# Optimization experiments

Measured on AMD Instinct MI355X. Metric: run time of the kernel, lower is better.

The kernel has to match this reference:

```python
import jax, jax.numpy as jnp
import numpy as np
import math

D_MODEL = 1024
NUM_HEADS = 16
HEAD_DIM = D_MODEL // NUM_HEADS
BATCH = 2
SEQ = 2048
THETA = 10000.0


def _rope_tables(seq_len, head_dim, theta=THETA):
    inv_freq = 1.0 / theta ** (jnp.arange(0, head_dim, 2, dtype=jnp.float32) / head_dim)
    pos = jnp.arange(seq_len, dtype=jnp.float32)
    freqs = jnp.outer(pos, inv_freq)                 # [S, hd/2]
    emb = jnp.concatenate([freqs, freqs], axis=-1)   # [S, hd]
    return jnp.cos(emb), jnp.sin(emb)


def _rotate_half(x):
    x1, x2 = jnp.split(x, 2, axis=-1)
    return jnp.concatenate([-x2, x1], axis=-1)


def setup_inputs() -> dict:
    key = jax.random.key(0)
    k1, k2, k3 = jax.random.split(key, 3)
    x = jax.random.normal(k1, (BATCH, SEQ, D_MODEL), dtype=jnp.float32)
    # causal mask: 1 where attend allowed, 0 where masked
    mask = jnp.tril(jnp.ones((SEQ, SEQ), dtype=jnp.int32))[None, None]
    w_qkv = jax.random.normal(k2, (D_MODEL, 3 * D_MODEL), dtype=jnp.float32) / math.sqrt(D_MODEL)
    w_out = jax.random.normal(k3, (D_MODEL, D_MODEL), dtype=jnp.float32) / math.sqrt(D_MODEL)
    return {"x": x, "mask": mask, "w_qkv": w_qkv, "w_out": w_out}


def reference(x, mask, w_qkv, w_out):
    B, S, _ = x.shape
    qkv = x @ w_qkv                                          # [B,S,3*D]
    qkv = qkv.reshape(B, S, 3, NUM_HEADS, HEAD_DIM)
    qkv = jnp.transpose(qkv, (2, 0, 3, 1, 4))                # [3,B,H,S,hd]
    q, k, v = qkv[0], qkv[1], qkv[2]
    cos, sin = _rope_tables(S, HEAD_DIM)                     # [S,hd]
    cos = cos[None, None]; sin = sin[None, None]
    q = q * cos + _rotate_half(q) * sin
    k = k * cos + _rotate_half(k) * sin
    scores = jnp.einsum('bhqd,bhkd->bhqk', q, k) / math.sqrt(HEAD_DIM)
    scores = jnp.where(mask == 0, -jnp.inf, scores)
    attn = jax.nn.softmax(scores, axis=-1)                   # dropout p=0 (eval)
    out = jnp.einsum('bhqk,bhkd->bhqd', attn, v)             # [B,H,S,hd]
    out = jnp.transpose(out, (0, 2, 1, 3)).reshape(B, S, D_MODEL)
    return out @ w_out
```

## Files before the change

### kernel.cpp

```cpp
#include <hip/hip_runtime.h>

typedef __bf16 bf16;
typedef __bf16 bf16x4 __attribute__((ext_vector_type(4)));
typedef __bf16 bf16x8 __attribute__((ext_vector_type(8)));
typedef float f32x4 __attribute__((ext_vector_type(4)));

constexpr int BATCH = 2;
constexpr int SEQ   = 2048;
constexpr int DMODEL= 1024;
constexpr int NH    = 16;
constexpr int HD    = 64;
constexpr int M_ROWS= BATCH * SEQ;
constexpr int N_QKV = 3 * DMODEL;

__device__ __forceinline__ void gl_lds16(const bf16* g, bf16* l) {
  __builtin_amdgcn_global_load_lds(
      (const __attribute__((address_space(1))) unsigned int*)g,
      (__attribute__((address_space(3))) unsigned int*)l, 16, 0, 0);
}

__global__ __launch_bounds__(256) void transpose_cast_kernel(
    const float* __restrict__ src, bf16* __restrict__ dst, int R, int C) {
  __shared__ float tile[32][33];
  const int c0 = blockIdx.x * 32, r0 = blockIdx.y * 32;
  const int tx = threadIdx.x, ty = threadIdx.y;
#pragma unroll
  for (int i = 0; i < 4; i++)
    tile[ty + 8 * i][tx] = src[(size_t)(r0 + ty + 8 * i) * C + c0 + tx];
  __syncthreads();
#pragma unroll
  for (int i = 0; i < 4; i++)
    dst[(size_t)(c0 + ty + 8 * i) * R + r0 + tx] = (bf16)tile[tx][ty + 8 * i];
}

__global__ __launch_bounds__(256) void cast_f32_bf16(
    const float* __restrict__ src, bf16* __restrict__ dst) {
  const int i = (blockIdx.x * 256 + threadIdx.x) * 8;
  float4 f0 = *(const float4*)&src[i];
  float4 f1 = *(const float4*)&src[i + 4];
  bf16x8 v;
  v[0] = (bf16)f0.x; v[1] = (bf16)f0.y; v[2] = (bf16)f0.z; v[3] = (bf16)f0.w;
  v[4] = (bf16)f1.x; v[5] = (bf16)f1.y; v[6] = (bf16)f1.z; v[7] = (bf16)f1.w;
  *(bf16x8*)&dst[i] = v;
}

#define GEMM_BODY(A, BT, K)                                                    \
  __shared__ bf16 As[128 * 32];                                                \
  __shared__ bf16 Bs[128 * 32];                                                \
  const int t = threadIdx.x;                                                   \
  const int m0 = blockIdx.y * 128;                                             \
  const int n0 = blockIdx.x * 128;                                             \
  const int w = t >> 6, lane = t & 63, g = lane >> 4, li = lane & 15;          \
  const int r0w = (w & 1) * 64, c0w = (w >> 1) * 64;                           \
  f32x4 acc[4][4] = {};                                                        \
  for (int k0 = 0; k0 < (K); k0 += 32) {                                       \
    __syncthreads();                                                           \
    _Pragma("unroll") for (int c = 0; c < 2; c++) {                            \
      const int idx = (w * 2 + c) * 64 + lane;                                 \
      const int row = idx >> 2, col = (idx & 3) * 8;                           \
      gl_lds16(&(A)[(size_t)(m0 + row) * (K) + k0 + col],                      \
               &As[(w * 2 + c) * 512]);                                        \
      gl_lds16(&(BT)[(size_t)(n0 + row) * (K) + k0 + col],                     \
               &Bs[(w * 2 + c) * 512]);                                        \
    }                                                                          \
    __syncthreads();                                                           \
    bf16x8 a[4], b[4];                                                         \
    _Pragma("unroll") for (int mt = 0; mt < 4; mt++)                           \
        a[mt] = *(const bf16x8*)&As[(r0w + mt * 16 + li) * 32 + g * 8];        \
    _Pragma("unroll") for (int nt = 0; nt < 4; nt++)                           \
        b[nt] = *(const bf16x8*)&Bs[(c0w + nt * 16 + li) * 32 + g * 8];        \
    _Pragma("unroll") for (int mt = 0; mt < 4; mt++)                           \
        _Pragma("unroll") for (int nt = 0; nt < 4; nt++)                       \
            acc[mt][nt] = __builtin_amdgcn_mfma_f32_16x16x32_bf16(             \
                a[mt], b[nt], acc[mt][nt], 0, 0, 0);                           \
  }

__global__ __launch_bounds__(256) void gemm_out(
    const bf16* __restrict__ A, const bf16* __restrict__ BT,
    float* __restrict__ C, int M, int N, int K) {
  GEMM_BODY(A, BT, K)
#pragma unroll
  for (int mt = 0; mt < 4; mt++)
#pragma unroll
    for (int nt = 0; nt < 4; nt++)
#pragma unroll
      for (int r = 0; r < 4; r++) {
        const int m = m0 + r0w + mt * 16 + g * 4 + r;
        const int n = n0 + c0w + nt * 16 + li;
        C[(size_t)m * N + n] = acc[mt][nt][r];
      }
}

__global__ __launch_bounds__(256) void gemm_qkv_rope(
    const bf16* __restrict__ A, const bf16* __restrict__ BT,
    bf16* __restrict__ Qb, bf16* __restrict__ Kb, bf16* __restrict__ Vt) {
  constexpr int K = DMODEL;
  GEMM_BODY(A, BT, K)

  const int region = n0 >> 10;
  const int b = m0 >> 11;
  const int h = ((n0 + c0w) >> 6) & 15;
  const size_t bh = (size_t)(b * NH + h);

  if (region < 2) {
    bf16* dst = region == 0 ? Qb : Kb;
    const float outsc = region == 0 ? 0.125f * 1.44269504f : 1.f;
    const float L = 13.287712379549449f;
    const float if0 = exp2f(-(float)(2 * li) / 64.f * L);
    const float if1 = exp2f(-(float)(2 * (li + 16)) / 64.f * L);
#pragma unroll
    for (int mt = 0; mt < 4; mt++)
#pragma unroll
      for (int r = 0; r < 4; r++) {
        const int s = (m0 + r0w + mt * 16 + g * 4 + r) & (SEQ - 1);
        float cs[2], sn[2];
        __sincosf((float)s * if0, &sn[0], &cs[0]);
        __sincosf((float)s * if1, &sn[1], &cs[1]);
#pragma unroll
        for (int nt = 0; nt < 4; nt++) {
          const int d = nt * 16 + li;
          const int par = nt & 1;
          const float a = acc[mt][nt][r];
          const float ap = acc[mt][nt ^ 2][r];
          const float v = (nt < 2) ? a * cs[par] - ap * sn[par]
                                   : a * cs[par] + ap * sn[par];
          dst[(bh * SEQ + s) * HD + d] = (bf16)(v * outsc);
        }
      }
  } else {
#pragma unroll
    for (int mt = 0; mt < 4; mt++)
#pragma unroll
      for (int nt = 0; nt < 4; nt++) {
        const int s = (m0 + r0w + mt * 16 + g * 4) & (SEQ - 1);
        const int d = nt * 16 + li;
        bf16x4 v;
#pragma unroll
        for (int r = 0; r < 4; r++) v[r] = (bf16)acc[mt][nt][r];
        *(bf16x4*)&Vt[(bh * HD + d) * SEQ + s] = v;
      }
  }
}

__global__ __launch_bounds__(512, 4) void flash_attn5(
    const bf16* __restrict__ Q, const bf16* __restrict__ Kb,
    const bf16* __restrict__ Vt, bf16* __restrict__ Oout) {
  const int f = blockIdx.x;
  const int c = f & 255, half = f >> 8;
  const int bh = c >> 3, idx = c & 7;
  const int qt = half ? 15 - idx : idx;
  const int q0 = qt * 128;
  const int t = threadIdx.x, w = t >> 6, lane = t & 63, g = lane >> 4,
            li = lane & 15;

  __shared__ bf16 Ks[2][4096];
  __shared__ bf16 Vs[2][4096];
  __shared__ bf16 Pl[8 * 1024];

  const bf16* Qh = Q  + (size_t)bh * SEQ * HD;
  const bf16* Kh = Kb + (size_t)bh * SEQ * HD;
  const bf16* Vh = Vt + (size_t)bh * HD * SEQ;

  const int qw = q0 + w * 16;

  bf16x8 qf[2];
#pragma unroll
  for (int ks = 0; ks < 2; ks++)
    qf[ks] = *(const bf16x8*)&Qh[(size_t)(qw + li) * HD + ks * 32 + g * 8];

  f32x4 o[4] = {};
  float l_[4] = {};

  const int p = w * 64 + lane;
  const int sr = p >> 3, sc = ((p & 7) ^ (sr & 7)) * 8;
  const int ldsoff = w * 512;

  const int jend = q0 + 128;
  gl_lds16(&Kh[(size_t)sr * HD + sc], &Ks[0][ldsoff]);
  gl_lds16(&Vh[(size_t)sr * SEQ + sc], &Vs[0][ldsoff]);
  __syncthreads();

  for (int j0 = 0; j0 < jend; j0 += 64) {
    const int cur = (j0 >> 6) & 1, nxt = cur ^ 1;
    if (j0 + 64 < jend) {
      const int jn = j0 + 64;
      gl_lds16(&Kh[(size_t)(jn + sr) * HD + sc], &Ks[nxt][ldsoff]);
      gl_lds16(&Vh[(size_t)sr * SEQ + jn + sc], &Vs[nxt][ldsoff]);
    }

    if (j0 <= qw + 15) {
      const bool masked = (j0 + 63 > qw);
      const int ntlim = masked ? ((qw + 15 - j0) >> 4) + 1 : 4;

      f32x4 sacc[4] = {};
#pragma unroll
      for (int ks = 0; ks < 2; ks++)
#pragma unroll
        for (int nt = 0; nt < 4; nt++) {
          if (nt >= ntlim) continue;
          const int rK = nt * 16 + li;
          const int pK = rK * 8 + ((ks * 4 + g) ^ (li & 7));
          bf16x8 kf = *(const bf16x8*)&Ks[cur][pK * 8];
          sacc[nt] = __builtin_amdgcn_mfma_f32_16x16x32_bf16(qf[ks], kf,
                                                             sacc[nt], 0, 0, 0);
        }

#pragma unroll
      for (int nt = 0; nt < 4; nt++)
#pragma unroll
        for (int r = 0; r < 4; r++) {
          const int row = g * 4 + r, col = nt * 16 + li;
          const int ch = row * 8 + ((col >> 3) ^ (row & 7));
          bf16 pv;
          if (nt < ntlim) {
            float v = sacc[nt][r];
            if (masked) v = (j0 + col <= qw + row) ? v : -1e30f;
            const float pe = exp2f(v);
            l_[r] += pe;
            pv = (bf16)pe;
          } else {
            pv = (bf16)0.f;
          }
          Pl[w * 1024 + ch * 8 + (col & 7)] = pv;
        }

      bf16x8 pf[2];
#pragma unroll
      for (int ks = 0; ks < 2; ks++) {
        const int pP = li * 8 + ((ks * 4 + g) ^ (li & 7));
        pf[ks] = *(const bf16x8*)&Pl[w * 1024 + pP * 8];
      }
#pragma unroll
      for (int ks = 0; ks < 2; ks++)
#pragma unroll
        for (int dt = 0; dt < 4; dt++) {
          const int rV = dt * 16 + li;
          const int pV = rV * 8 + ((ks * 4 + g) ^ (li & 7));
          bf16x8 vf = *(const bf16x8*)&Vs[cur][pV * 8];
          o[dt] = __builtin_amdgcn_mfma_f32_16x16x32_bf16(pf[ks], vf, o[dt],
                                                          0, 0, 0);
        }
    }
    __syncthreads();
  }

#pragma unroll
  for (int off = 1; off < 16; off <<= 1)
#pragma unroll
    for (int r = 0; r < 4; r++) l_[r] += __shfl_xor(l_[r], off, 64);

  const int b = bh >> 4, h = bh & 15;
#pragma unroll
  for (int dt = 0; dt < 4; dt++)
#pragma unroll
    for (int r = 0; r < 4; r++) {
      const int s = qw + g * 4 + r;
      const int d = dt * 16 + li;
      Oout[((size_t)(b * SEQ + s)) * DMODEL + h * 64 + d] =
          (bf16)(o[dt][r] / l_[r]);
    }
}

extern "C" void kernel_launch(void* const* d_in, const int* in_sizes, int n_in,
                              void* d_out, int out_size, void* d_ws,
                              size_t ws_size, hipStream_t stream) {
  const float* x     = (const float*)d_in[0];
  const float* w_qkv = (const float*)d_in[2];
  const float* w_out = (const float*)d_in[3];
  float* out = (float*)d_out;

  char* ws = (char*)d_ws;
  bf16* WqkvT = (bf16*)(ws);
  bf16* WoutT = (bf16*)(ws + 6291456);
  bf16* xb    = (bf16*)(ws + 8388608);
  bf16* Qb    = (bf16*)(ws + 16777216);
  bf16* Kbuf  = (bf16*)(ws + 25165824);
  bf16* Vt    = (bf16*)(ws + 33554432);
  bf16* attn  = (bf16*)(ws + 41943040);

  cast_f32_bf16<<<M_ROWS * DMODEL / 2048, 256, 0, stream>>>(x, xb);
  transpose_cast_kernel<<<dim3(N_QKV / 32, DMODEL / 32), dim3(32, 8), 0,
                          stream>>>(w_qkv, WqkvT, DMODEL, N_QKV);
  transpose_cast_kernel<<<dim3(DMODEL / 32, DMODEL / 32), dim3(32, 8), 0,
                          stream>>>(w_out, WoutT, DMODEL, DMODEL);
  gemm_qkv_rope<<<dim3(N_QKV / 128, M_ROWS / 128), 256, 0, stream>>>(
      xb, WqkvT, Qb, Kbuf, Vt);
  flash_attn5<<<dim3(512), 512, 0, stream>>>(Qb, Kbuf, Vt, attn);
  gemm_out<<<dim3(DMODEL / 128, M_ROWS / 128), 256, 0, stream>>>(
      attn, WoutT, out, M_ROWS, DMODEL, DMODEL);
}
```

Baseline: 230.0 us.

## Keep softmax probabilities in registers via transposed S MFMA, drop LDS P staging

```diff
diff --git a/kernel.cpp b/kernel.cpp
--- a/kernel.cpp
+++ b/kernel.cpp
@@ -3,6 +3,7 @@
 typedef __bf16 bf16;
 typedef __bf16 bf16x4 __attribute__((ext_vector_type(4)));
 typedef __bf16 bf16x8 __attribute__((ext_vector_type(8)));
+typedef short s16x4 __attribute__((ext_vector_type(4)));
 typedef float f32x4 __attribute__((ext_vector_type(4)));
 
 constexpr int BATCH = 2;
@@ -17,6 +18,16 @@
   __builtin_amdgcn_global_load_lds(
       (const __attribute__((address_space(1))) unsigned int*)g,
       (__attribute__((address_space(3))) unsigned int*)l, 16, 0, 0);
+}
+
+__device__ __forceinline__ f32x4 mfma_16x16x16_bf16(bf16x4 a, bf16x4 b,
+                                                    f32x4 c) {
+#if defined(__HIP_DEVICE_COMPILE__)
+  union { bf16x4 h; s16x4 s; } ua{a}, ub{b};
+  return __builtin_amdgcn_mfma_f32_16x16x16bf16_1k(ua.s, ub.s, c, 0, 0, 0);
+#else
+  return c;
+#endif
 }
 
 __global__ __launch_bounds__(256) void transpose_cast_kernel(
@@ -142,7 +153,7 @@
   }
 }
 
-__global__ __launch_bounds__(512, 4) void flash_attn5(
+__global__ __launch_bounds__(512, 4) void flash_attn6(
     const bf16* __restrict__ Q, const bf16* __restrict__ Kb,
     const bf16* __restrict__ Vt, bf16* __restrict__ Oout) {
   const int f = blockIdx.x;
@@ -155,7 +166,6 @@
 
   __shared__ bf16 Ks[2][4096];
   __shared__ bf16 Vs[2][4096];
-  __shared__ bf16 Pl[8 * 1024];
 
   const bf16* Qh = Q  + (size_t)bh * SEQ * HD;
   const bf16* Kh = Kb + (size_t)bh * SEQ * HD;
@@ -169,7 +179,7 @@
     qf[ks] = *(const bf16x8*)&Qh[(size_t)(qw + li) * HD + ks * 32 + g * 8];
 
   f32x4 o[4] = {};
-  float l_[4] = {};
+  float l_ = 0.f;
 
   const int p = w * 64 + lane;
   const int sr = p >> 3, sc = ((p & 7) ^ (sr & 7)) * 8;
@@ -190,7 +200,7 @@
 
     if (j0 <= qw + 15) {
       const bool masked = (j0 + 63 > qw);
-      const int ntlim = masked ? ((qw + 15 - j0) >> 4) + 1 : 4;
+      const int ntlim = min(4, ((qw + 15 - j0) >> 4) + 1);
 
       f32x4 sacc[4] = {};
 #pragma unroll
@@ -201,64 +211,57 @@
           const int rK = nt * 16 + li;
           const int pK = rK * 8 + ((ks * 4 + g) ^ (li & 7));
           bf16x8 kf = *(const bf16x8*)&Ks[cur][pK * 8];
-          sacc[nt] = __builtin_amdgcn_mfma_f32_16x16x32_bf16(qf[ks], kf,
+          sacc[nt] = __builtin_amdgcn_mfma_f32_16x16x32_bf16(kf, qf[ks],
                                                              sacc[nt], 0, 0, 0);
         }
 
-#pragma unroll
-      for (int nt = 0; nt < 4; nt++)
+      bf16x4 pf[4];
+#pragma unroll
+      for (int nt = 0; nt < 4; nt++) {
+        if (nt >= ntlim) continue;
 #pragma unroll
         for (int r = 0; r < 4; r++) {
-          const int row = g * 4 + r, col = nt * 16 + li;
-          const int ch = row * 8 + ((col >> 3) ^ (row & 7));
-          bf16 pv;
-          if (nt < ntlim) {
-            float v = sacc[nt][r];
-            if (masked) v = (j0 + col <= qw + row) ? v : -1e30f;
-            const float pe = exp2f(v);
-            l_[r] += pe;
-            pv = (bf16)pe;
-          } else {
-            pv = (bf16)0.f;
+          float v = sacc[nt][r];
+          if (masked) {
+            const int kk = j0 + nt * 16 + g * 4 + r;
+            v = (kk <= qw + li) ? v : -1e30f;
           }
-          Pl[w * 1024 + ch * 8 + (col & 7)] = pv;
-        }
-
-      bf16x8 pf[2];
-#pragma unroll
-      for (int ks = 0; ks < 2; ks++) {
-        const int pP = li * 8 + ((ks * 4 + g) ^ (li & 7));
-        pf[ks] = *(const bf16x8*)&Pl[w * 1024 + pP * 8];
-      }
-#pragma unroll
-      for (int ks = 0; ks < 2; ks++)
+          const float pe = exp2f(v);
+          l_ += pe;
+          pf[nt][r] = (bf16)pe;
+        }
+      }
+
+#pragma unroll
+      for (int nt = 0; nt < 4; nt++) {
+        if (nt >= ntlim) continue;
 #pragma unroll
         for (int dt = 0; dt < 4; dt++) {
           const int rV = dt * 16 + li;
-          const int pV = rV * 8 + ((ks * 4 + g) ^ (li & 7));
-          bf16x8 vf = *(const bf16x8*)&Vs[cur][pV * 8];
-          o[dt] = __builtin_amdgcn_mfma_f32_16x16x32_bf16(pf[ks], vf, o[dt],
-                                                          0, 0, 0);
-        }
+          const int cg = nt * 2 + (g >> 1);
+          const int pV = rV * 8 + (cg ^ (rV & 7));
+          bf16x4 vfrag = *(const bf16x4*)&Vs[cur][pV * 8 + (g & 1) * 4];
+          o[dt] = mfma_16x16x16_bf16(vfrag, pf[nt], o[dt]);
+        }
+      }
     }
     __syncthreads();
   }
 
-#pragma unroll
-  for (int off = 1; off < 16; off <<= 1)
-#pragma unroll
-    for (int r = 0; r < 4; r++) l_[r] += __shfl_xor(l_[r], off, 64);
+  l_ += __shfl_xor(l_, 16, 64);
+  l_ += __shfl_xor(l_, 32, 64);
+  const float inv_l = 1.f / l_;
 
   const int b = bh >> 4, h = bh & 15;
-#pragma unroll
-  for (int dt = 0; dt < 4; dt++)
-#pragma unroll
-    for (int r = 0; r < 4; r++) {
-      const int s = qw + g * 4 + r;
-      const int d = dt * 16 + li;
-      Oout[((size_t)(b * SEQ + s)) * DMODEL + h * 64 + d] =
-          (bf16)(o[dt][r] / l_[r]);
-    }
+  const int s = qw + li;
+#pragma unroll
+  for (int dt = 0; dt < 4; dt++) {
+    bf16x4 ov;
+#pragma unroll
+    for (int r = 0; r < 4; r++) ov[r] = (bf16)(o[dt][r] * inv_l);
+    *(bf16x4*)&Oout[((size_t)(b * SEQ + s)) * DMODEL + h * 64 + dt * 16 +
+                    g * 4] = ov;
+  }
 }
 
 extern "C" void kernel_launch(void* const* d_in, const int* in_sizes, int n_in,
@@ -285,7 +288,7 @@
                           stream>>>(w_out, WoutT, DMODEL, DMODEL);
   gemm_qkv_rope<<<dim3(N_QKV / 128, M_ROWS / 128), 256, 0, stream>>>(
       xb, WqkvT, Qb, Kbuf, Vt);
-  flash_attn5<<<dim3(512), 512, 0, stream>>>(Qb, Kbuf, Vt, attn);
+  flash_attn6<<<dim3(512), 512, 0, stream>>>(Qb, Kbuf, Vt, attn);
   gemm_out<<<dim3(DMODEL / 128, M_ROWS / 128), 256, 0, stream>>>(
       attn, WoutT, out, M_ROWS, DMODEL, DMODEL);
 }
```

New measurement: 220.1 us. -4.3%, faster.
